# Kernel tuning notes

Measured on AMD Instinct MI355X. Metric: run time of the kernel, lower is better.

Reference implementation:

```python
import jax, jax.numpy as jnp
import numpy as np

NUM_LEAF = 10000   # leaf classes
BRANCH = 100       # leaves per parent node
NUM_PARENTS = NUM_LEAF // BRANCH  # 100 internal parent nodes (+ 1 implicit root)
BATCH = 4096


def setup_inputs() -> dict:
    key = jax.random.key(0)
    k1, k2 = jax.random.split(key)
    inp = jax.random.normal(k1, (BATCH, NUM_LEAF), dtype=jnp.float32)
    target = jax.random.randint(k2, (BATCH,), 0, NUM_LEAF)
    # structural tensor: parent id of each leaf in the 2-level taxonomy
    leaf_parent = (jnp.arange(NUM_LEAF) // BRANCH).astype(jnp.int32)
    return {"input": inp, "target": target, "leaf_parent": leaf_parent}


def _bce_to_one(p):
    # BCELoss(reduction='sum') against all-ones targets: -log(p), with torch's
    # log clamp at -100, after clipping p into [0, 1] as the module does.
    p = jnp.clip(p, 0.0, 1.0)
    return jnp.minimum(-jnp.log(p), 100.0)


def reference(input, target, leaf_parent):
    probs = jax.nn.softmax(input, axis=1)                       # [B, L]
    # mapping-sum for every internal parent node, all samples at once:
    # parent_probs[b, p] = sum_{l: parent(l)==p} probs[b, l]
    parent_probs = jax.ops.segment_sum(
        probs.T, leaf_parent, num_segments=NUM_PARENTS).T       # [B, P]
    b = jnp.arange(probs.shape[0])
    leaf_p = probs[b, target]                                   # group = leaf itself
    par_p = parent_probs[b, leaf_parent[target]]                # group = parent(leaf)
    root_p = probs.sum(axis=1)                                  # group = root (all leaves)
    per_sample = _bce_to_one(leaf_p) + _bce_to_one(par_p) + _bce_to_one(root_p)
    return per_sample.mean()  # reduction='mean'
```

## Files before the change

### kernel.cpp

```cpp
#include <hip/hip_runtime.h>


#define NUM_LEAF 10000
#define BRANCH   100
#define BATCH    4096
#define NV4      (NUM_LEAF / 4)
#define WAVES_PER_BLOCK 4

typedef float vfloat4 __attribute__((ext_vector_type(4)));

__device__ __forceinline__ float exp_sum4(vfloat4 v) {
    return (__expf(v.x) + __expf(v.y)) + (__expf(v.z) + __expf(v.w));
}

__global__ __launch_bounds__(256) void hce_row_kernel(
    const float* __restrict__ input,
    const int*   __restrict__ target,
    const int*   __restrict__ leaf_parent,
    float*       __restrict__ row_loss)
{
    const int lane = threadIdx.x & 63;
    const int wave = threadIdx.x >> 6;
    const int row  = blockIdx.x * WAVES_PER_BLOCK + wave;

    const float*   x  = input + (size_t)row * NUM_LEAF;
    const vfloat4* x4 = (const vfloat4*)x;

    const int t  = target[row];
    const int p  = leaf_parent[t];
    const float xt = x[t];
    vfloat4 pv = {0.f, 0.f, 0.f, 0.f};
    if (lane < BRANCH / 4)
        pv = x4[p * (BRANCH / 4) + lane];

    float s0 = 0.f, s1 = 0.f, s2 = 0.f, s3 = 0.f;
    int i = lane;
    for (; i + 192 < NV4; i += 256) {
        vfloat4 a = __builtin_nontemporal_load(&x4[i]);
        vfloat4 b = __builtin_nontemporal_load(&x4[i +  64]);
        vfloat4 c = __builtin_nontemporal_load(&x4[i + 128]);
        vfloat4 d = __builtin_nontemporal_load(&x4[i + 192]);
        s0 += exp_sum4(a);
        s1 += exp_sum4(b);
        s2 += exp_sum4(c);
        s3 += exp_sum4(d);
    }
    for (; i < NV4; i += 64)
        s0 += exp_sum4(__builtin_nontemporal_load(&x4[i]));
    float s = (s0 + s1) + (s2 + s3);

    #pragma unroll
    for (int off = 32; off; off >>= 1) s += __shfl_down(s, off, 64);
    const float S = __shfl(s, 0, 64);

    float ps = 0.0f;
    if (lane < BRANCH / 4)
        ps = exp_sum4(pv);
    #pragma unroll
    for (int off = 32; off; off >>= 1) ps += __shfl_down(ps, off, 64);

    if (lane == 0) {
        const float lS = __logf(S);
        const float term_leaf = fminf(lS - xt,         100.0f);
        const float term_par  = fminf(lS - __logf(ps), 100.0f);
        row_loss[row] = term_leaf + term_par;
    }
}

__global__ __launch_bounds__(256) void hce_reduce_kernel(
    const float* __restrict__ row_loss, float* __restrict__ out)
{
    const int tid = threadIdx.x;
    float s = 0.0f;
    for (int i = tid; i < BATCH; i += 256) s += row_loss[i];
    #pragma unroll
    for (int off = 32; off; off >>= 1) s += __shfl_down(s, off, 64);

    __shared__ float wsum[4];
    if ((tid & 63) == 0) wsum[tid >> 6] = s;
    __syncthreads();
    if (tid == 0) out[0] = ((wsum[0] + wsum[1]) + (wsum[2] + wsum[3])) * (1.0f / BATCH);
}

extern "C" void kernel_launch(void* const* d_in, const int* in_sizes, int n_in,
                              void* d_out, int out_size, void* d_ws, size_t ws_size,
                              hipStream_t stream) {
    const float* input       = (const float*)d_in[0];
    const int*   target      = (const int*)d_in[1];
    const int*   leaf_parent = (const int*)d_in[2];
    float*       out         = (float*)d_out;
    float*       row_loss    = (float*)d_ws;

    hce_row_kernel<<<BATCH / WAVES_PER_BLOCK, 256, 0, stream>>>(
        input, target, leaf_parent, row_loss);
    hce_reduce_kernel<<<1, 256, 0, stream>>>(row_loss, out);
}
```

Measured before the change: 35.02 us.

## Split each softmax row across two waves and drop nontemporal loads

Each row's exp-sum is now split between two waves that each cover half of the row, with the partial sums combined through shared memory after a block barrier. The grid doubles to 2048 blocks of 2 rows each. The loads also switch from nontemporal to plain cached loads. The aim is more memory-level parallelism and shorter per-wave serial chains, at the cost of a __syncthreads and extra blocks.

```diff
diff --git a/kernel.cpp b/kernel.cpp
--- a/kernel.cpp
+++ b/kernel.cpp
@@ -5,7 +5,7 @@
 #define BRANCH   100
 #define BATCH    4096
 #define NV4      (NUM_LEAF / 4)
-#define WAVES_PER_BLOCK 4
+#define HALF4    (NV4 / 2)
 
 typedef float vfloat4 __attribute__((ext_vector_type(4)));
 
@@ -21,45 +21,58 @@
 {
     const int lane = threadIdx.x & 63;
     const int wave = threadIdx.x >> 6;
-    const int row  = blockIdx.x * WAVES_PER_BLOCK + wave;
+    const int half = wave & 1;
+    const int row  = blockIdx.x * 2 + (wave >> 1);
 
     const float*   x  = input + (size_t)row * NUM_LEAF;
     const vfloat4* x4 = (const vfloat4*)x;
 
-    const int t  = target[row];
-    const int p  = leaf_parent[t];
-    const float xt = x[t];
+    int t = 0, p = 0;
+    float xt = 0.f;
     vfloat4 pv = {0.f, 0.f, 0.f, 0.f};
-    if (lane < BRANCH / 4)
-        pv = x4[p * (BRANCH / 4) + lane];
+    if (half == 0) {
+        t  = target[row];
+        p  = leaf_parent[t];
+        xt = x[t];
+        if (lane < BRANCH / 4)
+            pv = x4[p * (BRANCH / 4) + lane];
+    }
 
+    const int start = half * HALF4;
+    const int end   = start + HALF4;
     float s0 = 0.f, s1 = 0.f, s2 = 0.f, s3 = 0.f;
-    int i = lane;
-    for (; i + 192 < NV4; i += 256) {
-        vfloat4 a = __builtin_nontemporal_load(&x4[i]);
-        vfloat4 b = __builtin_nontemporal_load(&x4[i +  64]);
-        vfloat4 c = __builtin_nontemporal_load(&x4[i + 128]);
-        vfloat4 d = __builtin_nontemporal_load(&x4[i + 192]);
+    int i = start + lane;
+    for (; i + 192 < end; i += 256) {
+        vfloat4 a = x4[i];
+        vfloat4 b = x4[i +  64];
+        vfloat4 c = x4[i + 128];
+        vfloat4 d = x4[i + 192];
         s0 += exp_sum4(a);
         s1 += exp_sum4(b);
         s2 += exp_sum4(c);
         s3 += exp_sum4(d);
     }
-    for (; i < NV4; i += 64)
-        s0 += exp_sum4(__builtin_nontemporal_load(&x4[i]));
+    for (; i < end; i += 64)
+        s0 += exp_sum4(x4[i]);
     float s = (s0 + s1) + (s2 + s3);
 
     #pragma unroll
     for (int off = 32; off; off >>= 1) s += __shfl_down(s, off, 64);
-    const float S = __shfl(s, 0, 64);
 
     float ps = 0.0f;
-    if (lane < BRANCH / 4)
-        ps = exp_sum4(pv);
-    #pragma unroll
-    for (int off = 32; off; off >>= 1) ps += __shfl_down(ps, off, 64);
+    if (half == 0) {
+        if (lane < BRANCH / 4)
+            ps = exp_sum4(pv);
+        #pragma unroll
+        for (int off = 32; off; off >>= 1) ps += __shfl_down(ps, off, 64);
+    }
 
-    if (lane == 0) {
+    __shared__ float hsum[4];
+    if (lane == 0) hsum[wave] = s;
+    __syncthreads();
+
+    if (half == 0 && lane == 0) {
+        const float S  = hsum[wave] + hsum[wave + 1];
         const float lS = __logf(S);
         const float term_leaf = fminf(lS - xt,         100.0f);
         const float term_par  = fminf(lS - __logf(ps), 100.0f);
@@ -91,7 +104,7 @@
     float*       out         = (float*)d_out;
     float*       row_loss    = (float*)d_ws;
 
-    hce_row_kernel<<<BATCH / WAVES_PER_BLOCK, 256, 0, stream>>>(
+    hce_row_kernel<<<BATCH / 2, 256, 0, stream>>>(
         input, target, leaf_parent, row_loss);
     hce_reduce_kernel<<<1, 256, 0, stream>>>(row_loss, out);
 }
```

Measured after the change: 35.75 us. 1.02x slower.
